# Optimization experiments

Measured on AMD Instinct MI355X. Metric: run time of the kernel, lower is better.

Reference implementation:

```python
import jax, jax.numpy as jnp
import numpy as np

GROUPS = 32
EPS = 1e-5

def group_norm(x, w, b):
    # x: [B, C, H, W]
    B, C, H, W = x.shape
    xg = x.reshape(B, GROUPS, C // GROUPS, H, W)
    mu = jnp.mean(xg, axis=(2, 3, 4), keepdims=True)
    var = jnp.var(xg, axis=(2, 3, 4), keepdims=True)
    xn = ((xg - mu) * jax.lax.rsqrt(var + EPS)).reshape(B, C, H, W)
    return xn * w[None, :, None, None] + b[None, :, None, None]

def setup_inputs() -> dict:
    key = jax.random.key(0)
    ks = jax.random.split(key, 6)
    B, C, H, W = 16, 512, 32, 32
    s = 1.0 / np.sqrt(C)  # conv1x1 fan-in init scale
    return {
        "x": jax.random.normal(ks[0], (B, C, H, W), jnp.float32),
        "gn_w": jnp.ones((C,), jnp.float32),
        "gn_b": jnp.zeros((C,), jnp.float32),
        "wq": jax.random.normal(ks[1], (C, C), jnp.float32) * s,
        "bq": jnp.zeros((C,), jnp.float32),
        "wk": jax.random.normal(ks[2], (C, C), jnp.float32) * s,
        "bk": jnp.zeros((C,), jnp.float32),
        "wv": jax.random.normal(ks[3], (C, C), jnp.float32) * s,
        "bv": jnp.zeros((C,), jnp.float32),
        "wp": jax.random.normal(ks[4], (C, C), jnp.float32) * s,
        "bp": jnp.zeros((C,), jnp.float32),
    }

def reference(x, gn_w, gn_b, wq, bq, wk, bk, wv, bv, wp, bp):
    B, C, H, W = x.shape
    h = group_norm(x, gn_w, gn_b)
    # 1x1 convs == per-pixel channel matmuls; tokens: [B, HW, C]
    ht = h.reshape(B, C, H * W).transpose(0, 2, 1)
    q = jnp.einsum('bnc,oc->bno', ht, wq) + bq
    k = jnp.einsum('bnc,oc->bno', ht, wk) + bk
    v = jnp.einsum('bnc,oc->bno', ht, wv) + bv
    scores = jnp.einsum('bnc,bmc->bnm', q, k) * (C ** -0.5)  # [B, HW, HW]
    attn = jax.nn.softmax(scores, axis=-1)
    o = jnp.einsum('bnm,bmc->bnc', attn, v)  # [B, HW, C]
    o = jnp.einsum('bnc,oc->bno', o, wp) + bp
    o = o.transpose(0, 2, 1).reshape(B, C, H, W)
    return x + o
```

## Files before the change

kernel.cpp:

```cpp
#include <hip/hip_runtime.h>
#include <hip/hip_bf16.h>


#define B_ 16
#define C_ 512
#define NTOK_ 1024
#define CPG_ 16
#define EPS_ 1e-5f
#define QSCALE_ 0.04419417382415922f

typedef __attribute__((ext_vector_type(8))) _Float16 f16x8;
typedef __attribute__((ext_vector_type(4))) float f32x4;
typedef const void __attribute__((address_space(1)))* gas1_t;
typedef void __attribute__((address_space(3)))* las3_t;

__device__ __forceinline__ ushort f2h(float x) {
    union { _Float16 h; ushort u; } c; c.h = (_Float16)x; return c.u;
}

__device__ __forceinline__ void gemm_core_f16(
    const ushort* __restrict__ A, int lda,
    const ushort* __restrict__ B, int ldb,
    int K, f32x4 acc[4][4])
{
    __shared__ alignas(16) char ldsc[32768];
    const int tid  = threadIdx.x;
    const int wave = tid >> 6, lane = tid & 63;
    const int wm = wave >> 1, wn = wave & 1;
    const int lrow = lane & 15, lk = lane >> 4;

    const int isB = wave >> 1;
    const ushort* P = isB ? B : A;
    const int ld = isB ? ldb : lda;
    const int sel = (lane & 7) ^ (lane >> 3);
    const int rowbase = ((wave & 1) << 6) + (lane >> 3);
    const ushort* src0 = P + (size_t)rowbase * ld + sel * 8;
    char* dst0 = ldsc + (isB << 14) + ((wave & 1) << 13);

    const int nsteps = K >> 6;
    for (int t = 0; t < nsteps; ++t) {
        const ushort* st = src0 + t * 64;
#pragma unroll
        for (int j = 0; j < 8; ++j) {
            __builtin_amdgcn_global_load_lds(
                (gas1_t)(st + (size_t)(j << 3) * ld),
                (las3_t)(dst0 + (j << 10)), 16, 0, 0);
        }
        __syncthreads();

        f16x8 af[4][2], bf[4][2];
#pragma unroll
        for (int m = 0; m < 4; ++m) {
            int row = wm * 64 + m * 16 + lrow;
            const char* base = ldsc + row * 128;
#pragma unroll
            for (int ks = 0; ks < 2; ++ks) {
                int c = ks * 4 + lk;
                af[m][ks] = *(const f16x8*)(base + ((c ^ (row & 7)) << 4));
            }
        }
#pragma unroll
        for (int n = 0; n < 4; ++n) {
            int row = wn * 64 + n * 16 + lrow;
            const char* base = ldsc + 16384 + row * 128;
#pragma unroll
            for (int ks = 0; ks < 2; ++ks) {
                int c = ks * 4 + lk;
                bf[n][ks] = *(const f16x8*)(base + ((c ^ (row & 7)) << 4));
            }
        }
#pragma unroll
        for (int m = 0; m < 4; ++m)
#pragma unroll
            for (int n = 0; n < 4; ++n) {
                acc[m][n] = __builtin_amdgcn_mfma_f32_16x16x32_f16(af[m][0], bf[n][0], acc[m][n], 0, 0, 0);
                acc[m][n] = __builtin_amdgcn_mfma_f32_16x16x32_f16(af[m][1], bf[n][1], acc[m][n], 0, 0, 0);
            }
        __syncthreads();
    }
}

#define ACC_ZERO(acc) do { \
    _Pragma("unroll") for (int m_ = 0; m_ < 4; ++m_) \
    _Pragma("unroll") for (int n_ = 0; n_ < 4; ++n_) \
        acc[m_][n_] = (f32x4){0.f, 0.f, 0.f, 0.f}; \
} while (0)

__global__ __launch_bounds__(256) void gn_stats_kernel(
    const float* __restrict__ x, const float* __restrict__ gw,
    const float* __restrict__ gb, float* __restrict__ scale_a,
    float* __restrict__ bias_a) {
    int bg = blockIdx.x;
    int b = bg >> 5, g = bg & 31;
    const float4* xp = (const float4*)(x + (size_t)(b * C_ + g * CPG_) * NTOK_);
    int tid = threadIdx.x;
    float s = 0.f, ss = 0.f;
    for (int i = tid; i < 4096; i += 256) {
        float4 v = xp[i];
        s += v.x + v.y + v.z + v.w;
        ss += v.x * v.x + v.y * v.y + v.z * v.z + v.w * v.w;
    }
    __shared__ float red[8];
    __shared__ float smu, srstd;
#pragma unroll
    for (int off = 32; off; off >>= 1) {
        s += __shfl_down(s, off);
        ss += __shfl_down(ss, off);
    }
    int wid = tid >> 6, lane = tid & 63;
    if (lane == 0) { red[wid] = s; red[wid + 4] = ss; }
    __syncthreads();
    if (tid == 0) {
        float S = red[0] + red[1] + red[2] + red[3];
        float SS = red[4] + red[5] + red[6] + red[7];
        float mu = S * (1.f / 16384.f);
        float var = SS * (1.f / 16384.f) - mu * mu;
        smu = mu;
        srstd = rsqrtf(var + EPS_);
    }
    __syncthreads();
    if (tid < CPG_) {
        int c = g * CPG_ + tid;
        float sc = srstd * gw[c];
        scale_a[b * C_ + c] = sc;
        bias_a[b * C_ + c] = gb[c] - smu * sc;
    }
}

__global__ __launch_bounds__(256) void prep_h_kernel(
    const float* __restrict__ x, const float* __restrict__ scale_a,
    const float* __restrict__ bias_a, ushort* __restrict__ h16) {
    __shared__ ushort sh[64][72];
    int tid = threadIdx.x;
    int ct = blockIdx.x, nt = blockIdx.y, b = blockIdx.z;
    int cl = tid >> 2, nq = tid & 3;
    int c = ct * 64 + cl;
    const float* xp = x + (((size_t)b * C_ + c) << 10) + nt * 64;
    float sc = scale_a[b * C_ + c], bi = bias_a[b * C_ + c];
#pragma unroll
    for (int i = 0; i < 4; ++i) {
        f32x4 v = *(const f32x4*)&xp[nq * 16 + i * 4];
#pragma unroll
        for (int j = 0; j < 4; ++j)
            sh[cl][nq * 16 + i * 4 + j] = f2h(v[j] * sc + bi);
    }
    __syncthreads();
    int nl = tid >> 2, cq = tid & 3;
    size_t ob = (((size_t)b << 10) + nt * 64 + nl) * C_ + ct * 64 + cq * 16;
    union { ushort u[8]; uint4 v; } p0, p1;
#pragma unroll
    for (int j = 0; j < 8; ++j) { p0.u[j] = sh[cq * 16 + j][nl]; p1.u[j] = sh[cq * 16 + 8 + j][nl]; }
    *(uint4*)&h16[ob] = p0.v;  *(uint4*)&h16[ob + 8] = p1.v;
}

__global__ __launch_bounds__(256) void prep_w_kernel(
    const float* __restrict__ wq, const float* __restrict__ wk,
    ushort* __restrict__ wq16, ushort* __restrict__ wk16) {
    int i = blockIdx.x * 256 + threadIdx.x;
    union { ushort u[4]; ushort4 v; } h;
    f32x4 a = ((const f32x4*)wq)[i];
#pragma unroll
    for (int j = 0; j < 4; ++j) h.u[j] = f2h(a[j]);
    ((ushort4*)wq16)[i] = h.v;
    f32x4 b = ((const f32x4*)wk)[i];
#pragma unroll
    for (int j = 0; j < 4; ++j) h.u[j] = f2h(b[j]);
    ((ushort4*)wk16)[i] = h.v;
}

__global__ __launch_bounds__(256) void weff_kernel(
    const float* __restrict__ wp, const float* __restrict__ wv,
    ushort* __restrict__ we16) {
    __shared__ float As[16][68], Bs[16][68];
    int tid = threadIdx.x, ty = tid >> 4, tx = tid & 15;
    int c0 = blockIdx.x << 6, p0 = blockIdx.y << 6;
    int a_row = tid >> 2, a_kq = tid & 3;
    int b_m = tid >> 4, b_cq = tid & 15;
    float acc[4][4] = {};
    for (int k0 = 0; k0 < C_; k0 += 16) {
        f32x4 a4 = *(const f32x4*)&wp[(size_t)(p0 + a_row) * C_ + k0 + a_kq * 4];
        As[a_kq * 4 + 0][a_row] = a4[0]; As[a_kq * 4 + 1][a_row] = a4[1];
        As[a_kq * 4 + 2][a_row] = a4[2]; As[a_kq * 4 + 3][a_row] = a4[3];
        *(f32x4*)&Bs[b_m][b_cq * 4] =
            *(const f32x4*)&wv[(size_t)(k0 + b_m) * C_ + c0 + b_cq * 4];
        __syncthreads();
#pragma unroll
        for (int kk = 0; kk < 16; ++kk) {
            f32x4 av = *(const f32x4*)&As[kk][ty << 2];
            f32x4 bv = *(const f32x4*)&Bs[kk][tx << 2];
#pragma unroll
            for (int i = 0; i < 4; ++i)
#pragma unroll
                for (int j = 0; j < 4; ++j) acc[i][j] += av[i] * bv[j];
        }
        __syncthreads();
    }
#pragma unroll
    for (int i = 0; i < 4; ++i) {
        union { ushort u[4]; ushort4 v; } hh;
#pragma unroll
        for (int j = 0; j < 4; ++j) hh.u[j] = f2h(acc[i][j]);
        *(ushort4*)&we16[(size_t)(p0 + ty * 4 + i) * C_ + c0 + tx * 4] = hh.v;
    }
}

__global__ __launch_bounds__(256) void bsum_kernel(
    const float* __restrict__ wp, const float* __restrict__ bv,
    const float* __restrict__ bp, float* __restrict__ bsum) {
    int p = blockIdx.x * 4 + (threadIdx.x >> 6);
    int lane = threadIdx.x & 63;
    const float* row = wp + (size_t)p * C_;
    f32x4 w0 = *(const f32x4*)&row[lane * 8];
    f32x4 w1 = *(const f32x4*)&row[lane * 8 + 4];
    f32x4 b0 = *(const f32x4*)&bv[lane * 8];
    f32x4 b1 = *(const f32x4*)&bv[lane * 8 + 4];
    float s = w0[0]*b0[0] + w0[1]*b0[1] + w0[2]*b0[2] + w0[3]*b0[3]
            + w1[0]*b1[0] + w1[1]*b1[1] + w1[2]*b1[2] + w1[3]*b1[3];
#pragma unroll
    for (int off = 32; off; off >>= 1) s += __shfl_down(s, off);
    if (lane == 0) bsum[p] = bp[p] + s;
}

__global__ __launch_bounds__(256) void gemm_qkv(
    const ushort* __restrict__ h16,
    const ushort* __restrict__ wq16, const ushort* __restrict__ wk16,
    const ushort* __restrict__ we16,
    const float* __restrict__ bq, const float* __restrict__ bk,
    ushort* __restrict__ q16, ushort* __restrict__ k16,
    ushort* __restrict__ vpt16) {
    int D = blockIdx.x + 12 * blockIdx.y;
    int L = ((D & 7) * 192) + (D >> 3);
    int lx = L % 12, mt = L / 12;
    int wsel = lx >> 2, ct = lx & 3;

    const ushort* Bw = wsel == 0 ? wq16 : (wsel == 1 ? wk16 : we16);
    const float* bias = wsel == 0 ? bq : bk;

    f32x4 acc[4][4]; ACC_ZERO(acc);
    gemm_core_f16(h16 + (size_t)mt * 128 * C_, C_,
                  Bw + (size_t)ct * 128 * C_, C_, C_, acc);

    int tid = threadIdx.x, wave = tid >> 6, lane = tid & 63;
    int wm = wave >> 1, wn = wave & 1, lrow = lane & 15, lk = lane >> 4;

    if (wsel < 2) {
        ushort* oh = wsel ? k16 : q16;
        float scale = wsel ? 1.f : QSCALE_;
#pragma unroll
        for (int mf = 0; mf < 4; ++mf) {
            int gm = mt * 128 + wm * 64 + mf * 16 + 4 * lk;
#pragma unroll
            for (int nf = 0; nf < 4; ++nf) {
                int gc = ct * 128 + wn * 64 + nf * 16 + lrow;
                float bi = bias[gc];
#pragma unroll
                for (int rg = 0; rg < 4; ++rg)
                    oh[(size_t)(gm + rg) * C_ + gc] = f2h((acc[mf][nf][rg] + bi) * scale);
            }
        }
    } else {
#pragma unroll
        for (int mf = 0; mf < 4; ++mf) {
            int gm0 = mt * 128 + wm * 64 + mf * 16 + 4 * lk;
            int b = gm0 >> 10, nl = gm0 & 1023;
#pragma unroll
            for (int nf = 0; nf < 4; ++nf) {
                int p = ct * 128 + wn * 64 + nf * 16 + lrow;
                union { ushort u[4]; ushort4 v; } hv;
#pragma unroll
                for (int rg = 0; rg < 4; ++rg) hv.u[rg] = f2h(acc[mf][nf][rg]);
                *(ushort4*)&vpt16[((size_t)b * C_ + p) * NTOK_ + nl] = hv.v;
            }
        }
    }
}

__global__ __launch_bounds__(256) void gemm_scores(
    const ushort* __restrict__ q16, const ushort* __restrict__ k16,
    float* __restrict__ s) {
    int D = blockIdx.x + (blockIdx.y << 3) + (blockIdx.z << 6);
    int L = ((D & 7) << 7) + (D >> 3);
    int nx = L & 7, my = (L >> 3) & 7, b = L >> 6;

    size_t ao = ((size_t)b * NTOK_ + my * 128) * C_;
    size_t bo = ((size_t)b * NTOK_ + nx * 128) * C_;
    f32x4 acc[4][4]; ACC_ZERO(acc);
    gemm_core_f16(q16 + ao, C_, k16 + bo, C_, C_, acc);

    int tid = threadIdx.x, wave = tid >> 6, lane = tid & 63;
    int wm = wave >> 1, wn = wave & 1, lrow = lane & 15, lk = lane >> 4;
#pragma unroll
    for (int mf = 0; mf < 4; ++mf) {
        int n = my * 128 + wm * 64 + mf * 16 + 4 * lk;
#pragma unroll
        for (int nf = 0; nf < 4; ++nf) {
            int m = nx * 128 + wn * 64 + nf * 16 + lrow;
#pragma unroll
            for (int rg = 0; rg < 4; ++rg)
                s[((size_t)b << 20) + (size_t)(n + rg) * NTOK_ + m] = acc[mf][nf][rg];
        }
    }
}

__global__ __launch_bounds__(256) void softmax_kernel(float* __restrict__ s) {
    size_t row = blockIdx.x;
    float* p = s + (row << 10);
    int tid = threadIdx.x;
    f32x4 v = *(const f32x4*)&p[tid * 4];
    __shared__ float redm[4], reds[4];
    float m = fmaxf(fmaxf(v[0], v[1]), fmaxf(v[2], v[3]));
#pragma unroll
    for (int off = 32; off; off >>= 1) m = fmaxf(m, __shfl_down(m, off));
    int wid = tid >> 6, lane = tid & 63;
    if (lane == 0) redm[wid] = m;
    __syncthreads();
    m = fmaxf(fmaxf(redm[0], redm[1]), fmaxf(redm[2], redm[3]));
#pragma unroll
    for (int j = 0; j < 4; ++j) v[j] = __expf(v[j] - m);
    float sum = v[0] + v[1] + v[2] + v[3];
#pragma unroll
    for (int off = 32; off; off >>= 1) sum += __shfl_down(sum, off);
    if (lane == 0) reds[wid] = sum;
    __syncthreads();
    float inv = 1.f / (reds[0] + reds[1] + reds[2] + reds[3]);
    union { ushort u[4]; ushort4 w; } hh;
#pragma unroll
    for (int j = 0; j < 4; ++j) hh.u[j] = f2h(v[j] * inv);
    ushort* bp8 = (ushort*)p;
    *(ushort4*)&bp8[tid * 4] = hh.w;
}

__global__ __launch_bounds__(256) void gemm_out(
    const float* __restrict__ s,
    const ushort* __restrict__ vpt16,
    const float* __restrict__ bsum, const float* __restrict__ x,
    float* __restrict__ out) {
    int D = blockIdx.x + (blockIdx.y << 2) + (blockIdx.z << 5);
    int L = ((D & 7) << 6) + (D >> 3);
    int ox = L & 3, ny = (L >> 2) & 7, b = L >> 5;

    const ushort* att = (const ushort*)s;
    const ushort* Ah = att + ((size_t)b * NTOK_ + ny * 128) * 2048;
    size_t bo = ((size_t)b * C_ + ox * 128) * NTOK_;
    f32x4 acc[4][4]; ACC_ZERO(acc);
    gemm_core_f16(Ah, 2048, vpt16 + bo, NTOK_, NTOK_, acc);

    int tid = threadIdx.x, wave = tid >> 6, lane = tid & 63;
    int wm = wave >> 1, wn = wave & 1, lrow = lane & 15, lk = lane >> 4;
#pragma unroll
    for (int mf = 0; mf < 4; ++mf) {
        int n0l = ny * 128 + wm * 64 + mf * 16 + 4 * lk;
#pragma unroll
        for (int nf = 0; nf < 4; ++nf) {
            int oc = ox * 128 + wn * 64 + nf * 16 + lrow;
            size_t base = ((size_t)b * C_ + oc) * NTOK_ + n0l;
            f32x4 xr = *(const f32x4*)&x[base];
            float bs = bsum[oc];
            f32x4 rv;
#pragma unroll
            for (int rg = 0; rg < 4; ++rg) rv[rg] = acc[mf][nf][rg] + bs + xr[rg];
            *(f32x4*)&out[base] = rv;
        }
    }
}

extern "C" void kernel_launch(void* const* d_in, const int* in_sizes, int n_in,
                              void* d_out, int out_size, void* d_ws, size_t ws_size,
                              hipStream_t stream) {
    const float* x  = (const float*)d_in[0];
    const float* gw = (const float*)d_in[1];
    const float* gb = (const float*)d_in[2];
    const float* wq = (const float*)d_in[3];
    const float* bq = (const float*)d_in[4];
    const float* wk = (const float*)d_in[5];
    const float* bk = (const float*)d_in[6];
    const float* wv = (const float*)d_in[7];
    const float* bv = (const float*)d_in[8];
    const float* wp = (const float*)d_in[9];
    const float* bp = (const float*)d_in[10];
    float* out = (float*)d_out;

    const size_t TOKC2 = (size_t)B_ * NTOK_ * C_ * 2;
    const size_t W2 = (size_t)C_ * C_ * 2;
    char* w = (char*)d_ws;
    auto carve = [&](size_t bytes) { char* p = w; w += (bytes + 255) & ~(size_t)255; return p; };

    float*  scale_a = (float*)carve(B_ * C_ * 4);
    float*  bias_a  = (float*)carve(B_ * C_ * 4);
    float*  bsumv   = (float*)carve(C_ * 4);
    ushort* h16     = (ushort*)carve(TOKC2);
    ushort* wq16    = (ushort*)carve(W2);
    ushort* wk16    = (ushort*)carve(W2);
    ushort* we16    = (ushort*)carve(W2);
    ushort* q16     = (ushort*)carve(TOKC2);
    ushort* k16     = (ushort*)carve(TOKC2);
    ushort* vpt16   = (ushort*)carve(TOKC2);
    float*  scores  = (float*)carve((size_t)B_ * NTOK_ * NTOK_ * 4);
    if ((size_t)(w - (char*)d_ws) > ws_size) return;

    gn_stats_kernel<<<B_ * 32, 256, 0, stream>>>(x, gw, gb, scale_a, bias_a);
    prep_h_kernel<<<dim3(8, 16, B_), 256, 0, stream>>>(x, scale_a, bias_a, h16);
    prep_w_kernel<<<256, 256, 0, stream>>>(wq, wk, wq16, wk16);
    weff_kernel<<<dim3(8, 8), 256, 0, stream>>>(wp, wv, we16);
    bsum_kernel<<<128, 256, 0, stream>>>(wp, bv, bp, bsumv);
    gemm_qkv<<<dim3(12, 128), 256, 0, stream>>>(h16, wq16, wk16, we16, bq, bk,
                                                q16, k16, vpt16);
    gemm_scores<<<dim3(8, 8, B_), 256, 0, stream>>>(q16, k16, scores);
    softmax_kernel<<<B_ * NTOK_, 256, 0, stream>>>(scores);
    gemm_out<<<dim3(4, 8, B_), 256, 0, stream>>>(scores, vpt16, bsumv, x, out);
}
```

Measured before the change: 256.7 us.

## Double-buffer GEMM LDS tiles and fuse group-norm stats with fp16 prep

The shared GEMM core now uses two LDS buffers. It prefetches the next K-tile with global_load_lds while MFMAs run on the current one, which removes the barrier between load and compute. The group-norm statistics kernel and the normalize/transpose-to-fp16 kernel are merged into one kernel. That kernel caches the group's 16 channels in LDS, so x is read once and the scale/bias scratch buffers go away. In exchange, the GEMM LDS footprint doubles to 64KB, which can lower occupancy. The fused prep kernel also uses about 66KB of LDS and writes 32-byte strided chunks per token.

```diff
diff --git a/kernel.cpp b/kernel.cpp
--- a/kernel.cpp
+++ b/kernel.cpp
@@ -23,7 +23,7 @@
     const ushort* __restrict__ B, int ldb,
     int K, f32x4 acc[4][4])
 {
-    __shared__ alignas(16) char ldsc[32768];
+    __shared__ alignas(16) char ldsc[2][32768];
     const int tid  = threadIdx.x;
     const int wave = tid >> 6, lane = tid & 63;
     const int wm = wave >> 1, wn = wave & 1;
@@ -35,24 +35,36 @@
     const int sel = (lane & 7) ^ (lane >> 3);
     const int rowbase = ((wave & 1) << 6) + (lane >> 3);
     const ushort* src0 = P + (size_t)rowbase * ld + sel * 8;
-    char* dst0 = ldsc + (isB << 14) + ((wave & 1) << 13);
+    const int dstoff = (isB << 14) + ((wave & 1) << 13);
 
     const int nsteps = K >> 6;
+
+#pragma unroll
+    for (int j = 0; j < 8; ++j) {
+        __builtin_amdgcn_global_load_lds(
+            (gas1_t)(src0 + (size_t)(j << 3) * ld),
+            (las3_t)(&ldsc[0][0] + dstoff + (j << 10)), 16, 0, 0);
+    }
+    __syncthreads();
+
     for (int t = 0; t < nsteps; ++t) {
-        const ushort* st = src0 + t * 64;
-#pragma unroll
-        for (int j = 0; j < 8; ++j) {
-            __builtin_amdgcn_global_load_lds(
-                (gas1_t)(st + (size_t)(j << 3) * ld),
-                (las3_t)(dst0 + (j << 10)), 16, 0, 0);
-        }
-        __syncthreads();
+        const char* cur = &ldsc[t & 1][0];
+        if (t + 1 < nsteps) {
+            const ushort* st = src0 + (t + 1) * 64;
+            char* nxt = &ldsc[(t + 1) & 1][0] + dstoff;
+#pragma unroll
+            for (int j = 0; j < 8; ++j) {
+                __builtin_amdgcn_global_load_lds(
+                    (gas1_t)(st + (size_t)(j << 3) * ld),
+                    (las3_t)(nxt + (j << 10)), 16, 0, 0);
+            }
+        }
 
         f16x8 af[4][2], bf[4][2];
 #pragma unroll
         for (int m = 0; m < 4; ++m) {
             int row = wm * 64 + m * 16 + lrow;
-            const char* base = ldsc + row * 128;
+            const char* base = cur + row * 128;
 #pragma unroll
             for (int ks = 0; ks < 2; ++ks) {
                 int c = ks * 4 + lk;
@@ -62,7 +74,7 @@
 #pragma unroll
         for (int n = 0; n < 4; ++n) {
             int row = wn * 64 + n * 16 + lrow;
-            const char* base = ldsc + 16384 + row * 128;
+            const char* base = cur + 16384 + row * 128;
 #pragma unroll
             for (int ks = 0; ks < 2; ++ks) {
                 int c = ks * 4 + lk;
@@ -86,22 +98,25 @@
         acc[m_][n_] = (f32x4){0.f, 0.f, 0.f, 0.f}; \
 } while (0)
 
-__global__ __launch_bounds__(256) void gn_stats_kernel(
+__global__ __launch_bounds__(256) void gn_prep_kernel(
     const float* __restrict__ x, const float* __restrict__ gw,
-    const float* __restrict__ gb, float* __restrict__ scale_a,
-    float* __restrict__ bias_a) {
+    const float* __restrict__ gb, ushort* __restrict__ h16) {
+    __shared__ float sx[16][1028];
+    __shared__ float red[8];
+    __shared__ float smu, srstd;
+    __shared__ float s_sc[16], s_bi[16];
     int bg = blockIdx.x;
     int b = bg >> 5, g = bg & 31;
-    const float4* xp = (const float4*)(x + (size_t)(b * C_ + g * CPG_) * NTOK_);
+    const float* xp = x + ((size_t)(b * C_ + g * CPG_) << 10);
     int tid = threadIdx.x;
     float s = 0.f, ss = 0.f;
     for (int i = tid; i < 4096; i += 256) {
-        float4 v = xp[i];
-        s += v.x + v.y + v.z + v.w;
-        ss += v.x * v.x + v.y * v.y + v.z * v.z + v.w * v.w;
-    }
-    __shared__ float red[8];
-    __shared__ float smu, srstd;
+        int c = i >> 8, n4 = (i & 255) << 2;
+        f32x4 v = *(const f32x4*)&xp[((size_t)c << 10) + n4];
+        *(f32x4*)&sx[c][n4] = v;
+        s += v[0] + v[1] + v[2] + v[3];
+        ss += v[0]*v[0] + v[1]*v[1] + v[2]*v[2] + v[3]*v[3];
+    }
 #pragma unroll
     for (int off = 32; off; off >>= 1) {
         s += __shfl_down(s, off);
@@ -122,35 +137,21 @@
     if (tid < CPG_) {
         int c = g * CPG_ + tid;
         float sc = srstd * gw[c];
-        scale_a[b * C_ + c] = sc;
-        bias_a[b * C_ + c] = gb[c] - smu * sc;
-    }
-}
-
-__global__ __launch_bounds__(256) void prep_h_kernel(
-    const float* __restrict__ x, const float* __restrict__ scale_a,
-    const float* __restrict__ bias_a, ushort* __restrict__ h16) {
-    __shared__ ushort sh[64][72];
-    int tid = threadIdx.x;
-    int ct = blockIdx.x, nt = blockIdx.y, b = blockIdx.z;
-    int cl = tid >> 2, nq = tid & 3;
-    int c = ct * 64 + cl;
-    const float* xp = x + (((size_t)b * C_ + c) << 10) + nt * 64;
-    float sc = scale_a[b * C_ + c], bi = bias_a[b * C_ + c];
-#pragma unroll
-    for (int i = 0; i < 4; ++i) {
-        f32x4 v = *(const f32x4*)&xp[nq * 16 + i * 4];
-#pragma unroll
-        for (int j = 0; j < 4; ++j)
-            sh[cl][nq * 16 + i * 4 + j] = f2h(v[j] * sc + bi);
-    }
-    __syncthreads();
-    int nl = tid >> 2, cq = tid & 3;
-    size_t ob = (((size_t)b << 10) + nt * 64 + nl) * C_ + ct * 64 + cq * 16;
-    union { ushort u[8]; uint4 v; } p0, p1;
-#pragma unroll
-    for (int j = 0; j < 8; ++j) { p0.u[j] = sh[cq * 16 + j][nl]; p1.u[j] = sh[cq * 16 + 8 + j][nl]; }
-    *(uint4*)&h16[ob] = p0.v;  *(uint4*)&h16[ob + 8] = p1.v;
+        s_sc[tid] = sc;
+        s_bi[tid] = gb[c] - smu * sc;
+    }
+    __syncthreads();
+#pragma unroll
+    for (int jn = 0; jn < 4; ++jn) {
+        int n = (tid << 2) + jn;
+        union { ushort u[16]; uint4 v[2]; } pk;
+#pragma unroll
+        for (int c = 0; c < 16; ++c)
+            pk.u[c] = f2h(sx[c][n] * s_sc[c] + s_bi[c]);
+        size_t ob = (((size_t)b << 10) + n) * C_ + g * CPG_;
+        *(uint4*)&h16[ob] = pk.v[0];
+        *(uint4*)&h16[ob + 8] = pk.v[1];
+    }
 }
 
 __global__ __launch_bounds__(256) void prep_w_kernel(
@@ -385,8 +386,6 @@
     char* w = (char*)d_ws;
     auto carve = [&](size_t bytes) { char* p = w; w += (bytes + 255) & ~(size_t)255; return p; };
 
-    float*  scale_a = (float*)carve(B_ * C_ * 4);
-    float*  bias_a  = (float*)carve(B_ * C_ * 4);
     float*  bsumv   = (float*)carve(C_ * 4);
     ushort* h16     = (ushort*)carve(TOKC2);
     ushort* wq16    = (ushort*)carve(W2);
@@ -398,8 +397,7 @@
     float*  scores  = (float*)carve((size_t)B_ * NTOK_ * NTOK_ * 4);
     if ((size_t)(w - (char*)d_ws) > ws_size) return;
 
-    gn_stats_kernel<<<B_ * 32, 256, 0, stream>>>(x, gw, gb, scale_a, bias_a);
-    prep_h_kernel<<<dim3(8, 16, B_), 256, 0, stream>>>(x, scale_a, bias_a, h16);
+    gn_prep_kernel<<<B_ * 32, 256, 0, stream>>>(x, gw, gb, h16);
     prep_w_kernel<<<256, 256, 0, stream>>>(wq, wk, wq16, wk16);
     weff_kernel<<<dim3(8, 8), 256, 0, stream>>>(wp, wv, we16);
     bsum_kernel<<<128, 256, 0, stream>>>(wp, bv, bp, bsumv);
```

New measurement: 252.7 us. Within noise of the previous version (-1.6%).
